# Performance work log

Measured on AMD Instinct MI355X. Metric: run time of the kernel, lower is better.

## Reference

```python
import jax, jax.numpy as jnp
import numpy as np

N = 32768   # points
C = 64      # channels (in == out, required by residual)
K = 16      # nsample
SP = 8      # share_planes
S = C // SP # attention channels per group
E = N * K


def _bn(t, g, b, eps=1e-5):
    # torch BatchNorm1d training-mode forward: biased batch variance
    m = t.mean(0)
    v = t.var(0)
    return (t - m) * jax.lax.rsqrt(v + eps) * g + b


def setup_inputs() -> dict:
    rng = np.random.default_rng(0)
    pos = (rng.standard_normal((N, 3)) * 10.0).astype(np.float32)
    # kNN graph (loop=True -> self is among the K nearest, distance 0), chunked
    sq = (pos ** 2).sum(1)
    nbr = np.empty((N, K), dtype=np.int64)
    chunk = 2048
    for s0 in range(0, N, chunk):
        s1 = min(s0 + chunk, N)
        d = sq[s0:s1, None] + sq[None, :] - 2.0 * (pos[s0:s1] @ pos.T)
        nbr[s0:s1] = np.argpartition(d, K - 1, axis=1)[:, :K]
    # PyG convention: edge_index[0]=source j (neighbor), edge_index[1]=target i
    edge_index = np.stack([nbr.reshape(-1),
                           np.repeat(np.arange(N, dtype=np.int64), K)])

    def lin_w(fo, fi):
        b = 1.0 / np.sqrt(fi)
        return jnp.asarray(rng.uniform(-b, b, size=(fo, fi)).astype(np.float32))

    def lin_b(fo, fi):
        b = 1.0 / np.sqrt(fi)
        return jnp.asarray(rng.uniform(-b, b, size=(fo,)).astype(np.float32))

    ones = lambda n: jnp.ones((n,), jnp.float32)
    zeros = lambda n: jnp.zeros((n,), jnp.float32)

    return {
        'pos': jnp.asarray(pos),
        'x': jnp.asarray(rng.standard_normal((N, C)).astype(np.float32)),
        'W1': lin_w(C, C),
        'Wk': lin_w(C, C), 'bk': lin_b(C, C),
        'Wq': lin_w(C, C), 'bq': lin_b(C, C),
        'Wv': lin_w(C, C), 'bv': lin_b(C, C),
        'p1_w': lin_w(3, 3), 'p1_b': lin_b(3, 3),
        'p_bn_g': ones(3), 'p_bn_b': zeros(3),
        'p2_w': lin_w(C, 3), 'p2_b': lin_b(C, 3),
        'w_bn1_g': ones(C), 'w_bn1_b': zeros(C),
        'w1_w': lin_w(S, C), 'w1_b': lin_b(S, C),
        'w_bn2_g': ones(S), 'w_bn2_b': zeros(S),
        'w2_w': lin_w(S, S), 'w2_b': lin_b(S, S),
        'W3': lin_w(C, C),
        'bn1_g': ones(C), 'bn1_b': zeros(C),
        'bn2_g': ones(C), 'bn2_b': zeros(C),
        'bn3_g': ones(C), 'bn3_b': zeros(C),
        'edge_index': jnp.asarray(edge_index),
    }


def reference(pos, x, W1, Wk, bk, Wq, bq, Wv, bv,
              p1_w, p1_b, p_bn_g, p_bn_b, p2_w, p2_b,
              w_bn1_g, w_bn1_b, w1_w, w1_b, w_bn2_g, w_bn2_b, w2_w, w2_b,
              W3, bn1_g, bn1_b, bn2_g, bn2_b, bn3_g, bn3_b, edge_index):
    x_skip = x
    h = jax.nn.relu(_bn(x @ W1.T, bn1_g, bn1_b))            # linear1 (no bias) + bn1 + relu

    # PointTransformerLayer
    k = h @ Wk.T + bk                                        # alpha_j source
    q = h @ Wq.T + bq                                        # alpha_i target
    v = h @ Wv.T + bv                                        # values
    src, dst = edge_index[0], edge_index[1]

    rel = pos[src] - pos[dst]                                # pos_j - pos_i  [E,3]
    delta = jax.nn.relu(_bn(rel @ p1_w.T + p1_b, p_bn_g, p_bn_b)) @ p2_w.T + p2_b  # [E,C]

    a = k[src] - q[dst] + delta                              # [E,C]
    a = jax.nn.relu(_bn(a, w_bn1_g, w_bn1_b)) @ w1_w.T + w1_b        # [E,S]
    a = jax.nn.relu(_bn(a, w_bn2_g, w_bn2_b)) @ w2_w.T + w2_b        # [E,S]

    # segment softmax over each target's neighborhood
    amax = jax.ops.segment_max(a, dst, num_segments=N)
    ae = jnp.exp(a - amax[dst])
    asum = jax.ops.segment_sum(ae, dst, num_segments=N)
    attn = ae / asum[dst]                                    # [E,S]

    # grouped weighted values: attn broadcast across the SP groups
    msg = (attn[:, None, :] * (v[src] + delta).reshape(E, SP, S)).reshape(E, C)
    out = jax.ops.segment_sum(msg, dst, num_segments=N)      # aggr='add' -> [N,C]

    h2 = jax.nn.relu(_bn(out, bn2_g, bn2_b))
    h3 = _bn(h2 @ W3.T, bn3_g, bn3_b)                        # linear3 (no bias) + bn3
    return jax.nn.relu(h3 + x_skip)
```

## Files before the change

kernel.cpp:

```cpp
#include <hip/hip_runtime.h>

#define NPTS 32768
#define CH 64
#define KNN 16
#define NE (NPTS*KNN)
#define EPS 1e-5f
#define NREP 32

#define G_P   0
#define G_BN1 (1*NREP*128)
#define G_W1  (2*NREP*128)
#define G_W2  (3*NREP*128)
#define G_BN2 (4*NREP*128)
#define G_BN3 (5*NREP*128)
#define STATS_FLOATS (6*NREP*128)

#define F_P   (STATS_FLOATS + 0*128)
#define F_BN1 (STATS_FLOATS + 1*128)
#define F_W1  (STATS_FLOATS + 2*128)
#define F_W2  (STATS_FLOATS + 3*128)
#define F_BN2 (STATS_FLOATS + 4*128)
#define F_BN3 (STATS_FLOATS + 5*128)

#define OFF_T1  (STATS_FLOATS + 1024)
#define SZ_NC   (NPTS*CH)
#define OFF_K   (OFF_T1 + SZ_NC)
#define OFF_Q   (OFF_K + SZ_NC)
#define OFF_V   (OFF_Q + SZ_NC)
#define OFF_A2  (OFF_V + SZ_NC)
#define OFF_OUT (OFF_A2 + NE*8)
#define OFF_U   (OFF_OUT + SZ_NC)
#define OFF_H3  OFF_U

__device__ __forceinline__ float frelu(float x){ return fmaxf(x, 0.f); }

__global__ __launch_bounds__(128) void k_fin(
    const float* __restrict__ gA, float invA, const float* __restrict__ gmA,
    const float* __restrict__ btA, float* __restrict__ outA, int nchA,
    const float* __restrict__ gB, float invB, const float* __restrict__ gmB,
    const float* __restrict__ btB, float* __restrict__ outB, int nchB)
{
    __shared__ float s_tmp[128];
    const int tid = threadIdx.x;
    const float* g; float inv; const float* gm; const float* bt; float* o; int nch;
    if (blockIdx.x == 0) { g=gA; inv=invA; gm=gmA; bt=btA; o=outA; nch=nchA; }
    else { if (!outB) return; g=gB; inv=invB; gm=gmB; bt=btB; o=outB; nch=nchB; }
    float t = 0.f;
    #pragma unroll
    for (int r=0;r<NREP;++r) t += g[r*128+tid];
    s_tmp[tid] = t;
    __syncthreads();
    if (tid < 64) {
        if (tid < nch) {
            float m = s_tmp[tid]*inv;
            float v = s_tmp[64+tid]*inv - m*m;
            float s = gm[tid]*rsqrtf(v+EPS);
            o[tid] = s; o[64+tid] = bt[tid] - m*s;
        } else { o[tid]=0.f; o[64+tid]=0.f; }
    }
}

__global__ __launch_bounds__(256) void k_pstats_u(
    const float* __restrict__ pos, const int* __restrict__ esrc,
    const float* __restrict__ p1w, const float* __restrict__ p1b,
    float4* __restrict__ u4, float* __restrict__ gstat)
{
    __shared__ float red[4][6];
    const int tid = threadIdx.x;
    const float w0=p1w[0],w1=p1w[1],w2=p1w[2],w3=p1w[3],w4=p1w[4],w5=p1w[5],w6=p1w[6],w7=p1w[7],w8=p1w[8];
    const float b0=p1b[0],b1=p1b[1],b2=p1b[2];
    const int e = blockIdx.x*256 + tid;
    const int sj = esrc[e]; const int d = e >> 4;
    float ax = pos[3*sj]-pos[3*d], ay = pos[3*sj+1]-pos[3*d+1], az = pos[3*sj+2]-pos[3*d+2];
    float u0 = w0*ax+w1*ay+w2*az+b0;
    float u1 = w3*ax+w4*ay+w5*az+b1;
    float u2 = w6*ax+w7*ay+w8*az+b2;
    u4[e] = make_float4(u0,u1,u2,0.f);
    float s0=u0,s1=u1,s2=u2,q0=u0*u0,q1=u1*u1,q2=u2*u2;
    #pragma unroll
    for (int m=32;m>=1;m>>=1){
        s0+=__shfl_xor(s0,m); s1+=__shfl_xor(s1,m); s2+=__shfl_xor(s2,m);
        q0+=__shfl_xor(q0,m); q1+=__shfl_xor(q1,m); q2+=__shfl_xor(q2,m);
    }
    const int wv = tid>>6;
    if ((tid&63)==0){ red[wv][0]=s0; red[wv][1]=s1; red[wv][2]=s2;
                      red[wv][3]=q0; red[wv][4]=q1; red[wv][5]=q2; }
    __syncthreads();
    float* g = gstat + (blockIdx.x & (NREP-1))*128;
    if (tid < 3)      atomicAdd(&g[tid],        red[0][tid]+red[1][tid]+red[2][tid]+red[3][tid]);
    else if (tid < 6) atomicAdd(&g[64+(tid-3)], red[0][tid]+red[1][tid]+red[2][tid]+red[3][tid]);
}

__global__ __launch_bounds__(256) void k_gemm64(
    const float* __restrict__ in, const float* __restrict__ W,
    float* __restrict__ out,
    const float* __restrict__ fbn, int applyBn,
    float* __restrict__ gstat)
{
    __shared__ float red[4][32];
    const int tid = threadIdx.x;
    const int wv = tid >> 6;
    const int by = blockIdx.x >> 7;
    const int rb = blockIdx.x & 127;
    const int c0 = by*16;
    const int row = rb*256 + tid;
    float xr[CH];
    {
        const float4* iv = (const float4*)(in + (size_t)row*CH);
        #pragma unroll
        for (int i=0;i<16;++i){ float4 t=iv[i];
            xr[4*i]=t.x; xr[4*i+1]=t.y; xr[4*i+2]=t.z; xr[4*i+3]=t.w; }
    }
    if (applyBn){
        #pragma unroll
        for (int i=0;i<CH;++i) xr[i] = frelu(xr[i]*fbn[i]+fbn[64+i]);
    }
    float4* ov = (float4*)(out + (size_t)row*CH + c0);
    #pragma unroll
    for (int q=0; q<4; ++q){
        float4 acc = make_float4(0,0,0,0);
        const float* wr0 = W + (size_t)(c0+q*4+0)*CH;
        const float* wr1 = W + (size_t)(c0+q*4+1)*CH;
        const float* wr2 = W + (size_t)(c0+q*4+2)*CH;
        const float* wr3 = W + (size_t)(c0+q*4+3)*CH;
        #pragma unroll
        for (int i=0;i<CH;++i){ float xv=xr[i];
            acc.x+=xv*wr0[i]; acc.y+=xv*wr1[i]; acc.z+=xv*wr2[i]; acc.w+=xv*wr3[i]; }
        ov[q]=acc;
        float4 sq = make_float4(acc.x*acc.x, acc.y*acc.y, acc.z*acc.z, acc.w*acc.w);
        #pragma unroll
        for (int m=32;m>=1;m>>=1){
            acc.x+=__shfl_xor(acc.x,m); acc.y+=__shfl_xor(acc.y,m);
            acc.z+=__shfl_xor(acc.z,m); acc.w+=__shfl_xor(acc.w,m);
            sq.x+=__shfl_xor(sq.x,m);  sq.y+=__shfl_xor(sq.y,m);
            sq.z+=__shfl_xor(sq.z,m);  sq.w+=__shfl_xor(sq.w,m);
        }
        if ((tid&63)==0){
            red[wv][q*4+0]=acc.x; red[wv][q*4+1]=acc.y; red[wv][q*4+2]=acc.z; red[wv][q*4+3]=acc.w;
            red[wv][16+q*4+0]=sq.x; red[wv][16+q*4+1]=sq.y; red[wv][16+q*4+2]=sq.z; red[wv][16+q*4+3]=sq.w;
        }
    }
    __syncthreads();
    if (tid < 32) {
        float t = red[0][tid]+red[1][tid]+red[2][tid]+red[3][tid];
        int dstc = (tid<16) ? (c0+tid) : (64 + c0 + (tid-16));
        atomicAdd(&gstat[(blockIdx.x & (NREP-1))*128 + dstc], t);
    }
}

__global__ __launch_bounds__(256) void k_kqv(
    const float* __restrict__ t1,
    const float* __restrict__ Wk, const float* __restrict__ bk,
    const float* __restrict__ Wq, const float* __restrict__ bq,
    const float* __restrict__ Wv, const float* __restrict__ bv,
    const float* __restrict__ fbn,
    float* __restrict__ kout, float* __restrict__ qout, float* __restrict__ vout)
{
    const int tid = threadIdx.x;
    const int m = blockIdx.x / 256;
    const int rem = blockIdx.x & 255;
    const int rb = rem >> 1;
    const int cbase = (rem & 1)*32;
    const float* W  = (m==0) ? Wk : (m==1 ? Wq : Wv);
    const float* bs = (m==0) ? bk : (m==1 ? bq : bv);
    float* o        = (m==0) ? kout : (m==1 ? qout : vout);

    const int row = rb*256 + tid;
    float h[CH];
    {
        const float4* iv = (const float4*)(t1 + (size_t)row*CH);
        #pragma unroll
        for (int i=0;i<16;++i){ float4 t=iv[i];
            h[4*i]=t.x; h[4*i+1]=t.y; h[4*i+2]=t.z; h[4*i+3]=t.w; }
    }
    #pragma unroll
    for (int i=0;i<CH;++i) h[i] = frelu(h[i]*fbn[i]+fbn[64+i]);

    float4* ov = (float4*)(o + (size_t)row*CH + cbase);
    #pragma unroll
    for (int q=0; q<8; ++q){
        float4 acc = make_float4(bs[cbase+q*4], bs[cbase+q*4+1], bs[cbase+q*4+2], bs[cbase+q*4+3]);
        const float* wr0 = W + (size_t)(cbase+q*4+0)*CH;
        const float* wr1 = W + (size_t)(cbase+q*4+1)*CH;
        const float* wr2 = W + (size_t)(cbase+q*4+2)*CH;
        const float* wr3 = W + (size_t)(cbase+q*4+3)*CH;
        #pragma unroll
        for (int i=0;i<CH;++i){ float xv=h[i];
            acc.x+=xv*wr0[i]; acc.y+=xv*wr1[i]; acc.z+=xv*wr2[i]; acc.w+=xv*wr3[i]; }
        ov[q]=acc;
    }
}

__global__ __launch_bounds__(256) void k_edge1(
    const int* __restrict__ esrc, const float4* __restrict__ u4,
    const float* __restrict__ kbuf, const float* __restrict__ qbuf,
    const float* __restrict__ fP,
    const float* __restrict__ p2w, const float* __restrict__ p2b,
    float* __restrict__ gstat)
{
    __shared__ float red[4][128];
    const int tid = threadIdx.x;
    const int c = tid & 63, wv = tid >> 6;
    const float scp0=fP[0], scp1=fP[1], scp2=fP[2];
    const float shp0=fP[64], shp1=fP[65], shp2=fP[66];
    const float w0 = p2w[c*3+0], w1 = p2w[c*3+1], w2 = p2w[c*3+2], bc = p2b[c];

    const int gw = blockIdx.x*4 + wv;
    const int chunk = NE/8192;
    const int e0 = gw*chunk;
    float s=0.f, q=0.f;
    #pragma unroll 4
    for (int e = e0; e < e0+chunk; ++e) {
        int sj = esrc[e]; int d = e >> 4;
        float4 uu = u4[e];
        float r0 = frelu(uu.x*scp0+shp0);
        float r1 = frelu(uu.y*scp1+shp1);
        float r2 = frelu(uu.z*scp2+shp2);
        float a = kbuf[(size_t)sj*CH+c] - qbuf[(size_t)d*CH+c]
                + (r0*w0 + r1*w1 + r2*w2 + bc);
        s += a; q += a*a;
    }
    red[wv][c] = s; red[wv][64+c] = q;
    __syncthreads();
    if (tid < 128) {
        float t = red[0][tid]+red[1][tid]+red[2][tid]+red[3][tid];
        atomicAdd(&gstat[(blockIdx.x & (NREP-1))*128 + tid], t);
    }
}

__global__ __launch_bounds__(256) void k_edge2(
    const int* __restrict__ esrc, const float4* __restrict__ u4,
    const float* __restrict__ kbuf, const float* __restrict__ qbuf,
    const float* __restrict__ fP,
    const float* __restrict__ p2w, const float* __restrict__ p2b,
    const float* __restrict__ fW1,
    const float* __restrict__ w1w, const float* __restrict__ w1bias,
    float* __restrict__ a2out, float* __restrict__ gstat)
{
    __shared__ float red[4][16];
    const int tid = threadIdx.x;
    const float scp0=fP[0], scp1=fP[1], scp2=fP[2];
    const float shp0=fP[64], shp1=fP[65], shp2=fP[66];

    const int e = blockIdx.x*256 + tid;
    const int sj = esrc[e]; const int d = e >> 4;
    float4 uu = u4[e];
    const float r0 = frelu(uu.x*scp0+shp0);
    const float r1 = frelu(uu.y*scp1+shp1);
    const float r2 = frelu(uu.z*scp2+shp2);
    const float4* kv = (const float4*)(kbuf + (size_t)sj*CH);
    const float4* qv = (const float4*)(qbuf + (size_t)d*CH);
    float a2a[8];
    #pragma unroll
    for (int j=0;j<8;++j) a2a[j] = w1bias[j];
    #pragma unroll
    for (int cc=0; cc<16; ++cc) {
        float4 k4 = kv[cc], q4 = qv[cc];
        const int c0 = cc*4;
        float b0 = frelu((k4.x - q4.x + r0*p2w[(c0+0)*3]+r1*p2w[(c0+0)*3+1]+r2*p2w[(c0+0)*3+2]+p2b[c0+0])*fW1[c0+0]+fW1[64+c0+0]);
        float b1 = frelu((k4.y - q4.y + r0*p2w[(c0+1)*3]+r1*p2w[(c0+1)*3+1]+r2*p2w[(c0+1)*3+2]+p2b[c0+1])*fW1[c0+1]+fW1[64+c0+1]);
        float b2 = frelu((k4.z - q4.z + r0*p2w[(c0+2)*3]+r1*p2w[(c0+2)*3+1]+r2*p2w[(c0+2)*3+2]+p2b[c0+2])*fW1[c0+2]+fW1[64+c0+2]);
        float b3 = frelu((k4.w - q4.w + r0*p2w[(c0+3)*3]+r1*p2w[(c0+3)*3+1]+r2*p2w[(c0+3)*3+2]+p2b[c0+3])*fW1[c0+3]+fW1[64+c0+3]);
        #pragma unroll
        for (int j=0;j<8;++j)
            a2a[j] += b0*w1w[j*64+c0] + b1*w1w[j*64+c0+1] + b2*w1w[j*64+c0+2] + b3*w1w[j*64+c0+3];
    }
    float4* a2v = (float4*)(a2out + (size_t)e*8);
    a2v[0] = make_float4(a2a[0],a2a[1],a2a[2],a2a[3]);
    a2v[1] = make_float4(a2a[4],a2a[5],a2a[6],a2a[7]);
    float q8[8];
    #pragma unroll
    for (int j=0;j<8;++j) q8[j]=a2a[j]*a2a[j];
    #pragma unroll
    for (int m=32;m>=1;m>>=1){
        #pragma unroll
        for (int j=0;j<8;++j){ a2a[j]+=__shfl_xor(a2a[j],m); q8[j]+=__shfl_xor(q8[j],m); }
    }
    const int wv = tid>>6;
    if ((tid&63)==0){
        #pragma unroll
        for (int j=0;j<8;++j){ red[wv][j]=a2a[j]; red[wv][8+j]=q8[j]; }
    }
    __syncthreads();
    if (tid < 16) {
        float t = red[0][tid]+red[1][tid]+red[2][tid]+red[3][tid];
        int dstc = (tid<8) ? tid : (64 + tid - 8);
        atomicAdd(&gstat[(blockIdx.x & (NREP-1))*128 + dstc], t);
    }
}

__global__ __launch_bounds__(256) void k_attn(
    const int* __restrict__ esrc, const float4* __restrict__ u4,
    const float* __restrict__ vbuf, const float* __restrict__ a2buf,
    const float* __restrict__ fP,
    const float* __restrict__ p2w, const float* __restrict__ p2b,
    const float* __restrict__ fW2,
    const float* __restrict__ w2w, const float* __restrict__ w2bias,
    float* __restrict__ outbuf, float* __restrict__ gstat)
{
    __shared__ float red[4][128];
    __shared__ float att[256][8];
    __shared__ float rrL[256][4];
    __shared__ int   sjL[256];
    const int tid = threadIdx.x;
    const float scp0=fP[0], scp1=fP[1], scp2=fP[2];
    const float shp0=fP[64], shp1=fP[65], shp2=fP[66];

    const int t = tid & 15;
    const int i = blockIdx.x*16 + (tid>>4);
    const int e = i*KNN + t;
    const int sj = esrc[e];
    sjL[tid] = sj;
    {
        float4 uu = u4[e];
        rrL[tid][0] = frelu(uu.x*scp0+shp0);
        rrL[tid][1] = frelu(uu.y*scp1+shp1);
        rrL[tid][2] = frelu(uu.z*scp2+shp2);
    }
    {
        const float4* a2v = (const float4*)a2buf;
        float4 aA = a2v[(size_t)e*2], aB = a2v[(size_t)e*2+1];
        float bb[8];
        bb[0]=frelu(aA.x*fW2[0]+fW2[64]); bb[1]=frelu(aA.y*fW2[1]+fW2[65]);
        bb[2]=frelu(aA.z*fW2[2]+fW2[66]); bb[3]=frelu(aA.w*fW2[3]+fW2[67]);
        bb[4]=frelu(aB.x*fW2[4]+fW2[68]); bb[5]=frelu(aB.y*fW2[5]+fW2[69]);
        bb[6]=frelu(aB.z*fW2[6]+fW2[70]); bb[7]=frelu(aB.w*fW2[7]+fW2[71]);
        float at[8];
        #pragma unroll
        for (int s=0;s<8;++s){
            float a3 = w2bias[s];
            #pragma unroll
            for (int u=0;u<8;++u) a3 += bb[u]*w2w[s*8+u];
            float m = a3;
            #pragma unroll
            for (int msk=8;msk>=1;msk>>=1) m = fmaxf(m, __shfl_xor(m,msk));
            float p = __expf(a3-m);
            float ssm = p;
            #pragma unroll
            for (int msk=8;msk>=1;msk>>=1) ssm += __shfl_xor(ssm,msk);
            at[s] = p/ssm;
        }
        ((float4*)att[tid])[0] = make_float4(at[0],at[1],at[2],at[3]);
        ((float4*)att[tid])[1] = make_float4(at[4],at[5],at[6],at[7]);
    }
    __syncthreads();
    const int base = (tid>>4)*16;
    const int c0 = 4*t;
    const int ho = (t&1);
    float pw[12], pbv[4];
    #pragma unroll
    for (int k2=0;k2<12;++k2) pw[k2] = p2w[c0*3+k2];
    #pragma unroll
    for (int k2=0;k2<4;++k2)  pbv[k2] = p2b[c0+k2];
    float4 res = make_float4(0,0,0,0);
    #pragma unroll 4
    for (int n=0; n<16; ++n){
        const int sjn = sjL[base+n];
        float4 v4 = ((const float4*)(vbuf + (size_t)sjn*CH))[t];
        const float rr0 = rrL[base+n][0], rr1 = rrL[base+n][1], rr2 = rrL[base+n][2];
        float4 a4 = ((const float4*)att[base+n])[ho];
        res.x += a4.x*(v4.x + rr0*pw[0]+rr1*pw[1]+rr2*pw[2]+pbv[0]);
        res.y += a4.y*(v4.y + rr0*pw[3]+rr1*pw[4]+rr2*pw[5]+pbv[1]);
        res.z += a4.z*(v4.z + rr0*pw[6]+rr1*pw[7]+rr2*pw[8]+pbv[2]);
        res.w += a4.w*(v4.w + rr0*pw[9]+rr1*pw[10]+rr2*pw[11]+pbv[3]);
    }
    ((float4*)outbuf)[(size_t)i*16 + t] = res;

    float4 sq = make_float4(res.x*res.x, res.y*res.y, res.z*res.z, res.w*res.w);
    #pragma unroll
    for (int msk=32;msk>=16;msk>>=1){
        res.x+=__shfl_xor(res.x,msk); res.y+=__shfl_xor(res.y,msk);
        res.z+=__shfl_xor(res.z,msk); res.w+=__shfl_xor(res.w,msk);
        sq.x+=__shfl_xor(sq.x,msk);  sq.y+=__shfl_xor(sq.y,msk);
        sq.z+=__shfl_xor(sq.z,msk);  sq.w+=__shfl_xor(sq.w,msk);
    }
    const int wv = tid>>6;
    if ((tid&63) < 16){
        red[wv][t*4+0]=res.x; red[wv][t*4+1]=res.y; red[wv][t*4+2]=res.z; red[wv][t*4+3]=res.w;
        red[wv][64+t*4+0]=sq.x; red[wv][64+t*4+1]=sq.y; red[wv][64+t*4+2]=sq.z; red[wv][64+t*4+3]=sq.w;
    }
    __syncthreads();
    if (tid < 128) {
        float tt = red[0][tid]+red[1][tid]+red[2][tid]+red[3][tid];
        atomicAdd(&gstat[(blockIdx.x & (NREP-1))*128 + tid], tt);
    }
}

__global__ __launch_bounds__(256) void k_final(
    const float* __restrict__ h3, const float* __restrict__ x,
    const float* __restrict__ fbn, float* __restrict__ out)
{
    const int tid = threadIdx.x;
    const int gi = blockIdx.x*256 + tid;
    const int c0 = (gi & 15)*4;
    float sc0=fbn[c0],sc1=fbn[c0+1],sc2=fbn[c0+2],sc3=fbn[c0+3];
    float sh0=fbn[64+c0],sh1=fbn[64+c0+1],sh2=fbn[64+c0+2],sh3=fbn[64+c0+3];
    float4 h = ((const float4*)h3)[gi];
    float4 xv = ((const float4*)x)[gi];
    float4 o;
    o.x = fmaxf(h.x*sc0+sh0+xv.x, 0.f);
    o.y = fmaxf(h.y*sc1+sh1+xv.y, 0.f);
    o.z = fmaxf(h.z*sc2+sh2+xv.z, 0.f);
    o.w = fmaxf(h.w*sc3+sh3+xv.w, 0.f);
    ((float4*)out)[gi] = o;
}

extern "C" void kernel_launch(void* const* d_in, const int* in_sizes, int n_in,
                              void* d_out, int out_size, void* d_ws, size_t ws_size,
                              hipStream_t stream) {
    (void)in_sizes; (void)n_in; (void)out_size; (void)ws_size;
    const float* pos   = (const float*)d_in[0];
    const float* x     = (const float*)d_in[1];
    const float* W1    = (const float*)d_in[2];
    const float* Wk    = (const float*)d_in[3];
    const float* bk    = (const float*)d_in[4];
    const float* Wq    = (const float*)d_in[5];
    const float* bq    = (const float*)d_in[6];
    const float* Wv    = (const float*)d_in[7];
    const float* bv    = (const float*)d_in[8];
    const float* p1w   = (const float*)d_in[9];
    const float* p1b   = (const float*)d_in[10];
    const float* pg    = (const float*)d_in[11];
    const float* pb    = (const float*)d_in[12];
    const float* p2w   = (const float*)d_in[13];
    const float* p2b   = (const float*)d_in[14];
    const float* w1g   = (const float*)d_in[15];
    const float* w1bb  = (const float*)d_in[16];
    const float* w1w   = (const float*)d_in[17];
    const float* w1bias= (const float*)d_in[18];
    const float* w2g   = (const float*)d_in[19];
    const float* w2bb  = (const float*)d_in[20];
    const float* w2w   = (const float*)d_in[21];
    const float* w2bias= (const float*)d_in[22];
    const float* W3    = (const float*)d_in[23];
    const float* bn1g  = (const float*)d_in[24];
    const float* bn1b  = (const float*)d_in[25];
    const float* bn2g  = (const float*)d_in[26];
    const float* bn2b  = (const float*)d_in[27];
    const float* bn3g  = (const float*)d_in[28];
    const float* bn3b  = (const float*)d_in[29];
    const int*   ei    = (const int*)d_in[30];
    float* ws  = (float*)d_ws;
    float* out = (float*)d_out;

    hipMemsetAsync(ws, 0, STATS_FLOATS*sizeof(float), stream);

    k_pstats_u<<<2048, 256, 0, stream>>>(pos, ei, p1w, p1b,
        (float4*)(ws+OFF_U), ws+G_P);
    k_gemm64<<<512, 256, 0, stream>>>(x, W1, ws+OFF_T1, nullptr, 0, ws+G_BN1);
    k_fin<<<2, 128, 0, stream>>>(ws+G_P, 1.f/NE, pg, pb, ws+F_P, 3,
                                 ws+G_BN1, 1.f/NPTS, bn1g, bn1b, ws+F_BN1, 64);
    k_kqv<<<768, 256, 0, stream>>>(ws+OFF_T1, Wk, bk, Wq, bq, Wv, bv,
        ws+F_BN1, ws+OFF_K, ws+OFF_Q, ws+OFF_V);
    k_edge1<<<2048, 256, 0, stream>>>(ei, (const float4*)(ws+OFF_U),
        ws+OFF_K, ws+OFF_Q, ws+F_P, p2w, p2b, ws+G_W1);
    k_fin<<<1, 128, 0, stream>>>(ws+G_W1, 1.f/NE, w1g, w1bb, ws+F_W1, 64,
                                 nullptr, 0.f, nullptr, nullptr, nullptr, 0);
    k_edge2<<<2048, 256, 0, stream>>>(ei, (const float4*)(ws+OFF_U),
        ws+OFF_K, ws+OFF_Q, ws+F_P, p2w, p2b,
        ws+F_W1, w1w, w1bias, ws+OFF_A2, ws+G_W2);
    k_fin<<<1, 128, 0, stream>>>(ws+G_W2, 1.f/NE, w2g, w2bb, ws+F_W2, 8,
                                 nullptr, 0.f, nullptr, nullptr, nullptr, 0);
    k_attn<<<2048, 256, 0, stream>>>(ei, (const float4*)(ws+OFF_U),
        ws+OFF_V, ws+OFF_A2, ws+F_P, p2w, p2b,
        ws+F_W2, w2w, w2bias, ws+OFF_OUT, ws+G_BN2);
    k_fin<<<1, 128, 0, stream>>>(ws+G_BN2, 1.f/NPTS, bn2g, bn2b, ws+F_BN2, 64,
                                 nullptr, 0.f, nullptr, nullptr, nullptr, 0);
    k_gemm64<<<512, 256, 0, stream>>>(ws+OFF_OUT, W3, ws+OFF_H3,
        ws+F_BN2, 1, ws+G_BN3);
    k_fin<<<1, 128, 0, stream>>>(ws+G_BN3, 1.f/NPTS, bn3g, bn3b, ws+F_BN3, 64,
                                 nullptr, 0.f, nullptr, nullptr, nullptr, 0);
    k_final<<<2048, 256, 0, stream>>>(ws+OFF_H3, x, ws+F_BN3, out);
}
```

Measured before the change: 325.7 us.

## Stage weights in LDS for GEMMs and split edge2 channels across 16 lanes

The two dense GEMM kernels (gemm64 and kqv) now stage a transposed 64x16 weight tile and the BN scale/shift in shared memory. Each thread streams its input row as float4 and accumulates 16 outputs, replacing the 64-float register array and the repeated global weight loads. kqv uses 16-column tiles and twice as many blocks, and edge1's per-warp chunk is halved with twice the grid. edge2 now spreads each edge over 16 lanes, each handling 4 channels, and combines partial dot products with shuffles. This raises parallelism and cuts per-thread register pressure, at the cost of extra shuffles and redundant index and pos loads per edge.

```diff
diff --git a/kernel.cpp b/kernel.cpp
--- a/kernel.cpp
+++ b/kernel.cpp
@@ -97,49 +97,60 @@
     const float* __restrict__ fbn, int applyBn,
     float* __restrict__ gstat)
 {
+    __shared__ float Wt[CH*16];
+    __shared__ float4 fL[32];
     __shared__ float red[4][32];
     const int tid = threadIdx.x;
     const int wv = tid >> 6;
     const int by = blockIdx.x >> 7;
     const int rb = blockIdx.x & 127;
     const int c0 = by*16;
+    #pragma unroll
+    for (int ch=0; ch<4; ++ch){
+        const int idx = ch*256 + tid;
+        Wt[idx] = W[(size_t)(c0 + (idx & 15))*CH + (idx >> 4)];
+    }
+    if (applyBn && tid < 32) fL[tid] = ((const float4*)fbn)[tid];
+    __syncthreads();
+
     const int row = rb*256 + tid;
-    float xr[CH];
-    {
-        const float4* iv = (const float4*)(in + (size_t)row*CH);
-        #pragma unroll
-        for (int i=0;i<16;++i){ float4 t=iv[i];
-            xr[4*i]=t.x; xr[4*i+1]=t.y; xr[4*i+2]=t.z; xr[4*i+3]=t.w; }
-    }
-    if (applyBn){
-        #pragma unroll
-        for (int i=0;i<CH;++i) xr[i] = frelu(xr[i]*fbn[i]+fbn[64+i]);
+    const float4* iv = (const float4*)(in + (size_t)row*CH);
+    const float4* Wt4 = (const float4*)Wt;
+    float4 a0 = make_float4(0,0,0,0), a1 = a0, a2 = a0, a3 = a0;
+    #pragma unroll
+    for (int j=0;j<16;++j){
+        float4 x4 = iv[j];
+        if (applyBn){
+            float4 s4 = fL[j], h4 = fL[16+j];
+            x4.x = frelu(x4.x*s4.x+h4.x); x4.y = frelu(x4.y*s4.y+h4.y);
+            x4.z = frelu(x4.z*s4.z+h4.z); x4.w = frelu(x4.w*s4.w+h4.w);
+        }
+        #define GSTEP(comp, xv) { \
+            float4 wq0 = Wt4[(4*j+comp)*4+0], wq1 = Wt4[(4*j+comp)*4+1]; \
+            float4 wq2 = Wt4[(4*j+comp)*4+2], wq3 = Wt4[(4*j+comp)*4+3]; \
+            a0.x += (xv)*wq0.x; a0.y += (xv)*wq0.y; a0.z += (xv)*wq0.z; a0.w += (xv)*wq0.w; \
+            a1.x += (xv)*wq1.x; a1.y += (xv)*wq1.y; a1.z += (xv)*wq1.z; a1.w += (xv)*wq1.w; \
+            a2.x += (xv)*wq2.x; a2.y += (xv)*wq2.y; a2.z += (xv)*wq2.z; a2.w += (xv)*wq2.w; \
+            a3.x += (xv)*wq3.x; a3.y += (xv)*wq3.y; a3.z += (xv)*wq3.z; a3.w += (xv)*wq3.w; }
+        GSTEP(0, x4.x) GSTEP(1, x4.y) GSTEP(2, x4.z) GSTEP(3, x4.w)
+        #undef GSTEP
     }
     float4* ov = (float4*)(out + (size_t)row*CH + c0);
-    #pragma unroll
-    for (int q=0; q<4; ++q){
-        float4 acc = make_float4(0,0,0,0);
-        const float* wr0 = W + (size_t)(c0+q*4+0)*CH;
-        const float* wr1 = W + (size_t)(c0+q*4+1)*CH;
-        const float* wr2 = W + (size_t)(c0+q*4+2)*CH;
-        const float* wr3 = W + (size_t)(c0+q*4+3)*CH;
-        #pragma unroll
-        for (int i=0;i<CH;++i){ float xv=xr[i];
-            acc.x+=xv*wr0[i]; acc.y+=xv*wr1[i]; acc.z+=xv*wr2[i]; acc.w+=xv*wr3[i]; }
-        ov[q]=acc;
-        float4 sq = make_float4(acc.x*acc.x, acc.y*acc.y, acc.z*acc.z, acc.w*acc.w);
-        #pragma unroll
-        for (int m=32;m>=1;m>>=1){
-            acc.x+=__shfl_xor(acc.x,m); acc.y+=__shfl_xor(acc.y,m);
-            acc.z+=__shfl_xor(acc.z,m); acc.w+=__shfl_xor(acc.w,m);
-            sq.x+=__shfl_xor(sq.x,m);  sq.y+=__shfl_xor(sq.y,m);
-            sq.z+=__shfl_xor(sq.z,m);  sq.w+=__shfl_xor(sq.w,m);
-        }
-        if ((tid&63)==0){
-            red[wv][q*4+0]=acc.x; red[wv][q*4+1]=acc.y; red[wv][q*4+2]=acc.z; red[wv][q*4+3]=acc.w;
-            red[wv][16+q*4+0]=sq.x; red[wv][16+q*4+1]=sq.y; red[wv][16+q*4+2]=sq.z; red[wv][16+q*4+3]=sq.w;
-        }
-    }
+    ov[0]=a0; ov[1]=a1; ov[2]=a2; ov[3]=a3;
+    #define STATQ(q, a) { \
+        float4 s = a; \
+        float4 sq = make_float4(s.x*s.x, s.y*s.y, s.z*s.z, s.w*s.w); \
+        _Pragma("unroll") \
+        for (int m=32;m>=1;m>>=1){ \
+            s.x+=__shfl_xor(s.x,m); s.y+=__shfl_xor(s.y,m); \
+            s.z+=__shfl_xor(s.z,m); s.w+=__shfl_xor(s.w,m); \
+            sq.x+=__shfl_xor(sq.x,m); sq.y+=__shfl_xor(sq.y,m); \
+            sq.z+=__shfl_xor(sq.z,m); sq.w+=__shfl_xor(sq.w,m); } \
+        if ((tid&63)==0){ \
+            red[wv][q*4+0]=s.x; red[wv][q*4+1]=s.y; red[wv][q*4+2]=s.z; red[wv][q*4+3]=s.w; \
+            red[wv][16+q*4+0]=sq.x; red[wv][16+q*4+1]=sq.y; red[wv][16+q*4+2]=sq.z; red[wv][16+q*4+3]=sq.w; } }
+    STATQ(0, a0) STATQ(1, a1) STATQ(2, a2) STATQ(3, a3)
+    #undef STATQ
     __syncthreads();
     if (tid < 32) {
         float t = red[0][tid]+red[1][tid]+red[2][tid]+red[3][tid];
@@ -156,39 +167,48 @@
     const float* __restrict__ fbn,
     float* __restrict__ kout, float* __restrict__ qout, float* __restrict__ vout)
 {
-    const int tid = threadIdx.x;
-    const int m = blockIdx.x / 256;
-    const int rem = blockIdx.x & 255;
-    const int rb = rem >> 1;
-    const int cbase = (rem & 1)*32;
+    __shared__ float Wt[CH*16];
+    __shared__ float4 fL[32];
+    __shared__ float4 bias4[4];
+    const int tid = threadIdx.x;
+    const int m = blockIdx.x / 512;
+    const int rem = blockIdx.x & 511;
+    const int rb = rem >> 2;
+    const int c0 = (rem & 3)*16;
     const float* W  = (m==0) ? Wk : (m==1 ? Wq : Wv);
     const float* bs = (m==0) ? bk : (m==1 ? bq : bv);
     float* o        = (m==0) ? kout : (m==1 ? qout : vout);
+    #pragma unroll
+    for (int ch=0; ch<4; ++ch){
+        const int idx = ch*256 + tid;
+        Wt[idx] = W[(size_t)(c0 + (idx & 15))*CH + (idx >> 4)];
+    }
+    if (tid < 32) fL[tid] = ((const float4*)fbn)[tid];
+    if (tid < 4)  bias4[tid] = ((const float4*)(bs + c0))[tid];
+    __syncthreads();
 
     const int row = rb*256 + tid;
-    float h[CH];
-    {
-        const float4* iv = (const float4*)(t1 + (size_t)row*CH);
-        #pragma unroll
-        for (int i=0;i<16;++i){ float4 t=iv[i];
-            h[4*i]=t.x; h[4*i+1]=t.y; h[4*i+2]=t.z; h[4*i+3]=t.w; }
-    }
-    #pragma unroll
-    for (int i=0;i<CH;++i) h[i] = frelu(h[i]*fbn[i]+fbn[64+i]);
-
-    float4* ov = (float4*)(o + (size_t)row*CH + cbase);
-    #pragma unroll
-    for (int q=0; q<8; ++q){
-        float4 acc = make_float4(bs[cbase+q*4], bs[cbase+q*4+1], bs[cbase+q*4+2], bs[cbase+q*4+3]);
-        const float* wr0 = W + (size_t)(cbase+q*4+0)*CH;
-        const float* wr1 = W + (size_t)(cbase+q*4+1)*CH;
-        const float* wr2 = W + (size_t)(cbase+q*4+2)*CH;
-        const float* wr3 = W + (size_t)(cbase+q*4+3)*CH;
-        #pragma unroll
-        for (int i=0;i<CH;++i){ float xv=h[i];
-            acc.x+=xv*wr0[i]; acc.y+=xv*wr1[i]; acc.z+=xv*wr2[i]; acc.w+=xv*wr3[i]; }
-        ov[q]=acc;
-    }
+    const float4* iv = (const float4*)(t1 + (size_t)row*CH);
+    const float4* Wt4 = (const float4*)Wt;
+    float4 a0 = bias4[0], a1 = bias4[1], a2 = bias4[2], a3 = bias4[3];
+    #pragma unroll
+    for (int j=0;j<16;++j){
+        float4 x4 = iv[j];
+        float4 s4 = fL[j], h4 = fL[16+j];
+        x4.x = frelu(x4.x*s4.x+h4.x); x4.y = frelu(x4.y*s4.y+h4.y);
+        x4.z = frelu(x4.z*s4.z+h4.z); x4.w = frelu(x4.w*s4.w+h4.w);
+        #define KSTEP(comp, xv) { \
+            float4 wq0 = Wt4[(4*j+comp)*4+0], wq1 = Wt4[(4*j+comp)*4+1]; \
+            float4 wq2 = Wt4[(4*j+comp)*4+2], wq3 = Wt4[(4*j+comp)*4+3]; \
+            a0.x += (xv)*wq0.x; a0.y += (xv)*wq0.y; a0.z += (xv)*wq0.z; a0.w += (xv)*wq0.w; \
+            a1.x += (xv)*wq1.x; a1.y += (xv)*wq1.y; a1.z += (xv)*wq1.z; a1.w += (xv)*wq1.w; \
+            a2.x += (xv)*wq2.x; a2.y += (xv)*wq2.y; a2.z += (xv)*wq2.z; a2.w += (xv)*wq2.w; \
+            a3.x += (xv)*wq3.x; a3.y += (xv)*wq3.y; a3.z += (xv)*wq3.z; a3.w += (xv)*wq3.w; }
+        KSTEP(0, x4.x) KSTEP(1, x4.y) KSTEP(2, x4.z) KSTEP(3, x4.w)
+        #undef KSTEP
+    }
+    float4* ov = (float4*)(o + (size_t)row*CH + c0);
+    ov[0]=a0; ov[1]=a1; ov[2]=a2; ov[3]=a3;
 }
 
 __global__ __launch_bounds__(256) void k_edge1(
@@ -206,7 +226,7 @@
     const float w0 = p2w[c*3+0], w1 = p2w[c*3+1], w2 = p2w[c*3+2], bc = p2b[c];
 
     const int gw = blockIdx.x*4 + wv;
-    const int chunk = NE/8192;
+    const int chunk = NE/16384;
     const int e0 = gw*chunk;
     float s=0.f, q=0.f;
     #pragma unroll 4
@@ -237,55 +257,68 @@
     const float* __restrict__ w1w, const float* __restrict__ w1bias,
     float* __restrict__ a2out, float* __restrict__ gstat)
 {
+    __shared__ float4 w1L[128];
     __shared__ float red[4][16];
     const int tid = threadIdx.x;
+    if (tid < 128) w1L[tid] = ((const float4*)w1w)[tid];
+    __syncthreads();
+
+    const int t = tid & 15;
+    const int e = blockIdx.x*16 + (tid >> 4);
+    const int sj = esrc[e]; const int d = e >> 4;
+    const int c0 = 4*t;
     const float scp0=fP[0], scp1=fP[1], scp2=fP[2];
     const float shp0=fP[64], shp1=fP[65], shp2=fP[66];
-
-    const int e = blockIdx.x*256 + tid;
-    const int sj = esrc[e]; const int d = e >> 4;
     float4 uu = u4[e];
     const float r0 = frelu(uu.x*scp0+shp0);
     const float r1 = frelu(uu.y*scp1+shp1);
     const float r2 = frelu(uu.z*scp2+shp2);
-    const float4* kv = (const float4*)(kbuf + (size_t)sj*CH);
-    const float4* qv = (const float4*)(qbuf + (size_t)d*CH);
-    float a2a[8];
-    #pragma unroll
-    for (int j=0;j<8;++j) a2a[j] = w1bias[j];
-    #pragma unroll
-    for (int cc=0; cc<16; ++cc) {
-        float4 k4 = kv[cc], q4 = qv[cc];
-        const int c0 = cc*4;
-        float b0 = frelu((k4.x - q4.x + r0*p2w[(c0+0)*3]+r1*p2w[(c0+0)*3+1]+r2*p2w[(c0+0)*3+2]+p2b[c0+0])*fW1[c0+0]+fW1[64+c0+0]);
-        float b1 = frelu((k4.y - q4.y + r0*p2w[(c0+1)*3]+r1*p2w[(c0+1)*3+1]+r2*p2w[(c0+1)*3+2]+p2b[c0+1])*fW1[c0+1]+fW1[64+c0+1]);
-        float b2 = frelu((k4.z - q4.z + r0*p2w[(c0+2)*3]+r1*p2w[(c0+2)*3+1]+r2*p2w[(c0+2)*3+2]+p2b[c0+2])*fW1[c0+2]+fW1[64+c0+2]);
-        float b3 = frelu((k4.w - q4.w + r0*p2w[(c0+3)*3]+r1*p2w[(c0+3)*3+1]+r2*p2w[(c0+3)*3+2]+p2b[c0+3])*fW1[c0+3]+fW1[64+c0+3]);
+    float4 k4 = ((const float4*)(kbuf + (size_t)sj*CH))[t];
+    float4 q4 = ((const float4*)(qbuf + (size_t)d*CH))[t];
+    float4 pb4 = ((const float4*)p2b)[t];
+    float4 sc4 = ((const float4*)fW1)[t];
+    float4 sh4 = ((const float4*)(fW1+64))[t];
+    float pw[12];
+    #pragma unroll
+    for (int k2=0;k2<12;++k2) pw[k2] = p2w[c0*3+k2];
+    const float b0 = frelu((k4.x - q4.x + r0*pw[0]+r1*pw[1]+r2*pw[2] +pb4.x)*sc4.x+sh4.x);
+    const float b1 = frelu((k4.y - q4.y + r0*pw[3]+r1*pw[4]+r2*pw[5] +pb4.y)*sc4.y+sh4.y);
+    const float b2 = frelu((k4.z - q4.z + r0*pw[6]+r1*pw[7]+r2*pw[8] +pb4.z)*sc4.z+sh4.z);
+    const float b3 = frelu((k4.w - q4.w + r0*pw[9]+r1*pw[10]+r2*pw[11]+pb4.w)*sc4.w+sh4.w);
+    float p[8];
+    #pragma unroll
+    for (int j=0;j<8;++j){
+        float4 w4 = w1L[j*16 + t];
+        p[j] = b0*w4.x + b1*w4.y + b2*w4.z + b3*w4.w;
+    }
+    #pragma unroll
+    for (int msk=8;msk>=1;msk>>=1){
         #pragma unroll
-        for (int j=0;j<8;++j)
-            a2a[j] += b0*w1w[j*64+c0] + b1*w1w[j*64+c0+1] + b2*w1w[j*64+c0+2] + b3*w1w[j*64+c0+3];
-    }
-    float4* a2v = (float4*)(a2out + (size_t)e*8);
-    a2v[0] = make_float4(a2a[0],a2a[1],a2a[2],a2a[3]);
-    a2v[1] = make_float4(a2a[4],a2a[5],a2a[6],a2a[7]);
-    float q8[8];
-    #pragma unroll
-    for (int j=0;j<8;++j) q8[j]=a2a[j]*a2a[j];
-    #pragma unroll
-    for (int m=32;m>=1;m>>=1){
+        for (int j=0;j<8;++j) p[j] += __shfl_xor(p[j], msk);
+    }
+    float a2f[8], sq[8];
+    #pragma unroll
+    for (int j=0;j<8;++j){ a2f[j] = p[j] + w1bias[j]; sq[j] = a2f[j]*a2f[j]; }
+    if (t < 2) {
+        float4 w = (t==0) ? make_float4(a2f[0],a2f[1],a2f[2],a2f[3])
+                          : make_float4(a2f[4],a2f[5],a2f[6],a2f[7]);
+        ((float4*)a2out)[(size_t)e*2 + t] = w;
+    }
+    #pragma unroll
+    for (int msk=32;msk>=16;msk>>=1){
         #pragma unroll
-        for (int j=0;j<8;++j){ a2a[j]+=__shfl_xor(a2a[j],m); q8[j]+=__shfl_xor(q8[j],m); }
+        for (int j=0;j<8;++j){ a2f[j]+=__shfl_xor(a2f[j],msk); sq[j]+=__shfl_xor(sq[j],msk); }
     }
     const int wv = tid>>6;
     if ((tid&63)==0){
         #pragma unroll
-        for (int j=0;j<8;++j){ red[wv][j]=a2a[j]; red[wv][8+j]=q8[j]; }
+        for (int j=0;j<8;++j){ red[wv][j]=a2f[j]; red[wv][8+j]=sq[j]; }
     }
     __syncthreads();
     if (tid < 16) {
-        float t = red[0][tid]+red[1][tid]+red[2][tid]+red[3][tid];
+        float tt = red[0][tid]+red[1][tid]+red[2][tid]+red[3][tid];
         int dstc = (tid<8) ? tid : (64 + tid - 8);
-        atomicAdd(&gstat[(blockIdx.x & (NREP-1))*128 + dstc], t);
+        atomicAdd(&gstat[(blockIdx.x & (NREP-1))*128 + dstc], tt);
     }
 }
 
@@ -450,13 +483,13 @@
     k_gemm64<<<512, 256, 0, stream>>>(x, W1, ws+OFF_T1, nullptr, 0, ws+G_BN1);
     k_fin<<<2, 128, 0, stream>>>(ws+G_P, 1.f/NE, pg, pb, ws+F_P, 3,
                                  ws+G_BN1, 1.f/NPTS, bn1g, bn1b, ws+F_BN1, 64);
-    k_kqv<<<768, 256, 0, stream>>>(ws+OFF_T1, Wk, bk, Wq, bq, Wv, bv,
+    k_kqv<<<1536, 256, 0, stream>>>(ws+OFF_T1, Wk, bk, Wq, bq, Wv, bv,
         ws+F_BN1, ws+OFF_K, ws+OFF_Q, ws+OFF_V);
-    k_edge1<<<2048, 256, 0, stream>>>(ei, (const float4*)(ws+OFF_U),
+    k_edge1<<<4096, 256, 0, stream>>>(ei, (const float4*)(ws+OFF_U),
         ws+OFF_K, ws+OFF_Q, ws+F_P, p2w, p2b, ws+G_W1);
     k_fin<<<1, 128, 0, stream>>>(ws+G_W1, 1.f/NE, w1g, w1bb, ws+F_W1, 64,
                                  nullptr, 0.f, nullptr, nullptr, nullptr, 0);
-    k_edge2<<<2048, 256, 0, stream>>>(ei, (const float4*)(ws+OFF_U),
+    k_edge2<<<32768, 256, 0, stream>>>(ei, (const float4*)(ws+OFF_U),
         ws+OFF_K, ws+OFF_Q, ws+F_P, p2w, p2b,
         ws+F_W1, w1w, w1bias, ws+OFF_A2, ws+G_W2);
     k_fin<<<1, 128, 0, stream>>>(ws+G_W2, 1.f/NE, w2g, w2bb, ws+F_W2, 8,
```

New measurement: 585.6 us. 79.8% more time.
